# Kernel tuning notes

Measured on AMD Instinct MI355X. Metric: run time of the kernel, lower is better.

The kernel has to match this reference:

```python
import jax, jax.numpy as jnp
import numpy as np

NEG = jnp.float32(-1e9)


def setup_inputs() -> dict:
    key = jax.random.key(0)
    ks = jax.random.split(key, 8)
    B, S, D = 8, 2048, 1024
    scale = 1.0 / np.sqrt(D)
    return {
        "xQ": jax.random.normal(ks[0], (B, S, D), jnp.float32),
        "xK": jax.random.normal(ks[1], (B, S, D), jnp.float32),
        "xV": jax.random.normal(ks[2], (B, S, D), jnp.float32),
        "padding_mask": jax.random.randint(ks[3], (B, S), 0, 2, jnp.int32),
        "casual_mask": jnp.ones((B, S), jnp.int32),
        "W_q": jax.random.normal(ks[4], (D, D), jnp.float32) * scale,
        "b_q": jnp.zeros((D,), jnp.float32),
        "W_k": jax.random.normal(ks[5], (D, D), jnp.float32) * scale,
        "b_k": jnp.zeros((D,), jnp.float32),
        "W_v": jax.random.normal(ks[6], (D, D), jnp.float32) * scale,
        "b_v": jnp.zeros((D,), jnp.float32),
    }


def reference(xQ, xK, xV, padding_mask, casual_mask, W_q, b_q, W_k, b_k, W_v, b_v):
    # Linear projections (torch nn.Linear: x @ W.T + b)
    Q = jnp.einsum('bsd,ed->bse', xQ, W_q) + b_q
    K = jnp.einsum('bsd,ed->bse', xK, W_k) + b_k
    V = jnp.einsum('bsd,ed->bse', xV, W_v) + b_v

    # Raw logits (note: original code applies NO 1/sqrt(dk) scaling)
    QKT = jnp.einsum('bqd,bkd->bqk', Q, K)  # [B, Sq, Sk]

    # Additive padding mask: -1e9 on padded key positions
    pad = jnp.where(padding_mask[:, None, :] == 0, NEG, jnp.float32(0.0))
    # Additive causal mask: -1e9 above the diagonal
    Sq, Sk = QKT.shape[1], QKT.shape[2]
    caus = jnp.where(
        jnp.tril(jnp.ones((Sq, Sk), dtype=bool)), jnp.float32(0.0), NEG
    )[None, :, :]
    QKT = QKT + pad + caus

    S = jax.nn.softmax(QKT, axis=-1)
    return jnp.einsum('bqk,bkd->bqd', S, V)
```

## Files before the change

kernel.cpp:

```cpp
#include <hip/hip_runtime.h>

typedef __attribute__((ext_vector_type(4))) float f4;
typedef __attribute__((ext_vector_type(4))) float f32x4;
typedef _Float16 half8 __attribute__((ext_vector_type(8)));

#define DEVI static __device__ __forceinline__

DEVI void gload_lds16(const void* g, void* l) {
  __builtin_amdgcn_global_load_lds(
      (const __attribute__((address_space(1))) void*)g,
      (__attribute__((address_space(3))) void*)l, 16, 0, 0);
}

DEVI int xcd_swz(int id, int n) {
  int q = n >> 3, r = n & 7;
  int x = id & 7, c = id >> 3;
  return (x < r ? x * (q + 1) : r * (q + 1) + (x - r) * q) + c;
}

#define FENCED_BARRIER()                \
  __builtin_amdgcn_sched_barrier(0);    \
  __builtin_amdgcn_s_barrier();         \
  __builtin_amdgcn_sched_barrier(0);

#define SWZ(kgv, rowv) ((((kgv) ^ ((rowv) >> 1)) & 3) * 8)

__global__ __launch_bounds__(256) void cvt_plain(const float* __restrict__ X,
                                                 _Float16* __restrict__ H,
                                                 int n4) {
  int i = blockIdx.x * 256 + threadIdx.x;
  const int stride = gridDim.x * 256;
  typedef _Float16 half4v __attribute__((ext_vector_type(4)));
  for (; i < n4; i += stride) {
    f4 x = ((const f4*)X)[i];
    half4v h;
#pragma unroll
    for (int j = 0; j < 4; ++j) h[j] = (_Float16)x[j];
    ((half4v*)H)[i] = h;
  }
}

__global__ __launch_bounds__(256) void cvt_split(const float* __restrict__ X,
                                                 _Float16* __restrict__ H,
                                                 _Float16* __restrict__ L,
                                                 int n4) {
  int i = blockIdx.x * 256 + threadIdx.x;
  const int stride = gridDim.x * 256;
  typedef _Float16 half4v __attribute__((ext_vector_type(4)));
  for (; i < n4; i += stride) {
    f4 x = ((const f4*)X)[i];
    half4v h, l;
#pragma unroll
    for (int j = 0; j < 4; ++j) {
      h[j] = (_Float16)x[j];
      l[j] = (_Float16)(x[j] - (float)h[j]);
    }
    ((half4v*)H)[i] = h;
    ((half4v*)L)[i] = l;
  }
}

DEVI void acc_zero44(f32x4 (&acc)[4][4]) {
#pragma unroll
  for (int i = 0; i < 4; ++i)
#pragma unroll
    for (int j = 0; j < 4; ++j) acc[i][j] = (f32x4)0.0f;
}
DEVI void acc_zero42(f32x4 (&acc)[4][2]) {
#pragma unroll
  for (int i = 0; i < 4; ++i)
#pragma unroll
    for (int j = 0; j < 2; ++j) acc[i][j] = (f32x4)0.0f;
}

template <int WSPLIT, int OUTMODE>
__global__ __launch_bounds__(512, 2) void proj_fused(
    const float* __restrict__ X, const _Float16* __restrict__ Wh,
    const _Float16* __restrict__ Wl, const float* __restrict__ bias,
    _Float16* __restrict__ OutHi, _Float16* __restrict__ OutLo,
    _Float16* __restrict__ VtOut) {
  extern __shared__ _Float16 lds[];
  constexpr int ACH = 256 * 32;
  constexpr int BCH = 128 * 32;
  constexpr int CHUNK = ACH + BCH * (1 + WSPLIT);
  const int id = xcd_swz(blockIdx.x, gridDim.x);
  const int m0 = (id >> 3) * 256, n0 = (id & 7) * 128;
  const float* A = X + (size_t)m0 * 1024;
  const _Float16* B0 = Wh + (size_t)n0 * 1024;
  const _Float16* B1 = Wl + (size_t)n0 * 1024;
  const int tid = threadIdx.x;
  const int w = tid >> 6, lane = tid & 63;
  const int wm = w >> 1, wn = w & 1;
  const int r16 = lane & 15, kg = lane >> 4;
  f32x4 acc[4][4];
  acc_zero44(acc);
  f4 ra[4];

  auto ALOAD = [&](int t) {
#pragma unroll
    for (int j = 0; j < 2; ++j) {
      int g = tid + j * 512;
      int row = g >> 2, c = g & 3;
      const float* src = A + (size_t)row * 1024 + t * 32 + c * 8;
      ra[2 * j] = *(const f4*)src;
      ra[2 * j + 1] = *(const f4*)(src + 4);
    }
  };
  auto AWRITE = [&](int buf) {
    _Float16* ab = lds + buf * CHUNK;
#pragma unroll
    for (int j = 0; j < 2; ++j) {
      int g = tid + j * 512;
      int row = g >> 2, c = g & 3;
      half8 h;
#pragma unroll
      for (int e = 0; e < 4; ++e) {
        h[e] = (_Float16)ra[2 * j][e];
        h[e + 4] = (_Float16)ra[2 * j + 1][e];
      }
      *(half8*)(ab + (size_t)row * 32 + SWZ(c, row)) = h;
    }
  };
  auto WLOAD = [&](int t, int buf) {
    _Float16* bb = lds + buf * CHUNK + ACH;
    int row = tid >> 2, c = tid & 3;
    int cs = (c ^ (row >> 1)) & 3;
    gload_lds16(B0 + (size_t)row * 1024 + t * 32 + cs * 8, bb + tid * 8);
    if (WSPLIT)
      gload_lds16(B1 + (size_t)row * 1024 + t * 32 + cs * 8,
                  bb + BCH + tid * 8);
  };
  auto COMPUTE = [&](int buf) {
    const _Float16* la = lds + buf * CHUNK;
    const _Float16* lb = la + ACH;
    half8 a[4], b0f[4], b1f[4];
#pragma unroll
    for (int mi = 0; mi < 4; ++mi) {
      int row = wm * 64 + mi * 16 + r16;
      a[mi] = *(const half8*)(la + row * 32 + SWZ(kg, row));
    }
#pragma unroll
    for (int ni = 0; ni < 4; ++ni) {
      int row = wn * 64 + ni * 16 + r16;
      int off = row * 32 + SWZ(kg, row);
      b0f[ni] = *(const half8*)(lb + off);
      if (WSPLIT) b1f[ni] = *(const half8*)(lb + BCH + off);
    }
    __builtin_amdgcn_s_setprio(1);
#pragma unroll
    for (int mi = 0; mi < 4; ++mi)
#pragma unroll
      for (int ni = 0; ni < 4; ++ni) {
        acc[mi][ni] = __builtin_amdgcn_mfma_f32_16x16x32_f16(
            a[mi], b0f[ni], acc[mi][ni], 0, 0, 0);
        if (WSPLIT)
          acc[mi][ni] = __builtin_amdgcn_mfma_f32_16x16x32_f16(
              a[mi], b1f[ni], acc[mi][ni], 0, 0, 0);
      }
    __builtin_amdgcn_s_setprio(0);
  };

  const int NS = 32;
  WLOAD(0, 0);
  ALOAD(0);
  asm volatile("s_waitcnt vmcnt(0)" ::: "memory");
  __builtin_amdgcn_sched_barrier(0);
  AWRITE(0);
  asm volatile("s_waitcnt lgkmcnt(0)" ::: "memory");
  FENCED_BARRIER();
  for (int t = 0; t < NS; ++t) {
    if (t + 1 < NS) {
      WLOAD(t + 1, (t + 1) & 1);
      ALOAD(t + 1);
    }
    COMPUTE(t & 1);
    if (t + 1 < NS) {
      asm volatile("s_waitcnt vmcnt(0)" ::: "memory");
      __builtin_amdgcn_sched_barrier(0);
      AWRITE((t + 1) & 1);
      asm volatile("s_waitcnt lgkmcnt(0)" ::: "memory");
      FENCED_BARRIER();
    }
  }

  float bcol[4];
#pragma unroll
  for (int ni = 0; ni < 4; ++ni) bcol[ni] = bias[n0 + wn * 64 + ni * 16 + r16];

  if (OUTMODE != 2) {
#pragma unroll
    for (int mi = 0; mi < 4; ++mi) {
      int row = m0 + wm * 64 + mi * 16 + kg * 4;
#pragma unroll
      for (int ni = 0; ni < 4; ++ni) {
        int col = n0 + wn * 64 + ni * 16 + r16;
#pragma unroll
        for (int j = 0; j < 4; ++j) {
          float v = acc[mi][ni][j] + bcol[ni];
          _Float16 h = (_Float16)v;
          OutHi[(size_t)(row + j) * 1024 + col] = h;
          if (OUTMODE == 0)
            OutLo[(size_t)(row + j) * 1024 + col] = (_Float16)(v - (float)h);
        }
      }
    }
  } else {
    __syncthreads();
    _Float16(*T)[256] = (_Float16(*)[256])lds;
#pragma unroll
    for (int mi = 0; mi < 4; ++mi) {
      int ml = wm * 64 + mi * 16 + kg * 4;
#pragma unroll
      for (int ni = 0; ni < 4; ++ni) {
        int nl = wn * 64 + ni * 16 + r16;
#pragma unroll
        for (int j = 0; j < 4; ++j)
          T[nl][ml + j] = (_Float16)(acc[mi][ni][j] + bcol[ni]);
      }
    }
    __syncthreads();
    const int b = m0 >> 11;
    const int s0 = m0 & 2047;
#pragma unroll
    for (int r = 0; r < 8; ++r) {
      int flat = tid + r * 512;
      int n = flat >> 5, c = flat & 31;
      half8 v = *(const half8*)&T[n][c * 8];
      *(half8*)(VtOut + (size_t)b * (1024 * 2048) + (size_t)(n0 + n) * 2048 +
                s0 + c * 8) = v;
    }
  }
}

__global__ __launch_bounds__(512, 4) void qk_eng(
    const _Float16* __restrict__ Qh, const _Float16* __restrict__ Ql,
    const _Float16* __restrict__ Kh, float* __restrict__ Lg, int bbase) {
  extern __shared__ _Float16 lds[];
  constexpr int CHUNK = 12288;
  const int id = xcd_swz(blockIdx.x, gridDim.x);
  const int y = id / 144;
  int t = id % 144;
  int g4 = 0, base = 0;
  while (t >= base + (g4 + 1) * 4) { base += (g4 + 1) * 4; ++g4; }
  const int rem = t - base;
  const int qt = g4 * 4 + rem / (g4 + 1);
  const int kt = rem % (g4 + 1);
  const int b = bbase + y;
  const size_t boff = (size_t)b * (2048 * 1024);
  const _Float16* A0 = Qh + boff + (size_t)(qt * 64) * 1024;
  const _Float16* A1 = Ql + boff + (size_t)(qt * 64) * 1024;
  const _Float16* B0 = Kh + boff + (size_t)(kt * 256) * 1024;
  const int tid = threadIdx.x;
  const int w = tid >> 6, lane = tid & 63;
  const int r16 = lane & 15, kg = lane >> 4;
  const int wn = w;
  f32x4 acc[4][2];
  acc_zero42(acc);

  auto STAGE = [&](int t_, int buf) {
    _Float16* base_ = lds + buf * CHUNK;
    {
      int g = tid & 255;
      int row = g >> 2, c = g & 3;
      int cs = (c ^ (row >> 1)) & 3;
      const _Float16* src = (tid < 256) ? A0 : A1;
      _Float16* dst = base_ + ((tid < 256) ? 0 : 2048);
      gload_lds16(src + (size_t)row * 1024 + t_ * 32 + cs * 8, dst + g * 8);
    }
#pragma unroll
    for (int j = 0; j < 2; ++j) {
      int g = tid + j * 512;
      int row = g >> 2, c = g & 3;
      int cs = (c ^ (row >> 1)) & 3;
      gload_lds16(B0 + (size_t)row * 1024 + t_ * 32 + cs * 8,
                  base_ + 4096 + g * 8);
    }
  };
  auto COMPUTE = [&](int buf) {
    const _Float16* la = lds + buf * CHUNK;
    half8 a0[4], a1[4], bf[2];
#pragma unroll
    for (int mi = 0; mi < 4; ++mi) {
      int row = mi * 16 + r16;
      int off = row * 32 + SWZ(kg, row);
      a0[mi] = *(const half8*)(la + off);
      a1[mi] = *(const half8*)(la + 2048 + off);
    }
#pragma unroll
    for (int ni = 0; ni < 2; ++ni) {
      int row = wn * 32 + ni * 16 + r16;
      bf[ni] = *(const half8*)(la + 4096 + row * 32 + SWZ(kg, row));
    }
    __builtin_amdgcn_s_setprio(1);
#pragma unroll
    for (int mi = 0; mi < 4; ++mi)
#pragma unroll
      for (int ni = 0; ni < 2; ++ni) {
        acc[mi][ni] = __builtin_amdgcn_mfma_f32_16x16x32_f16(
            a0[mi], bf[ni], acc[mi][ni], 0, 0, 0);
        acc[mi][ni] = __builtin_amdgcn_mfma_f32_16x16x32_f16(
            a1[mi], bf[ni], acc[mi][ni], 0, 0, 0);
      }
    __builtin_amdgcn_s_setprio(0);
  };

  const int NS = 32;
  STAGE(0, 0);
  STAGE(1, 1);
  int tt = 0;
  for (; tt < NS - 1; ++tt) {
    asm volatile("s_waitcnt vmcnt(3)" ::: "memory");
    FENCED_BARRIER();
    if (tt + 2 < NS) STAGE(tt + 2, (tt + 2) % 3);
    COMPUTE(tt % 3);
  }
  asm volatile("s_waitcnt vmcnt(0)" ::: "memory");
  FENCED_BARRIER();
  COMPUTE(tt % 3);

  float* L = Lg + (size_t)y * (2048 * 2048);
#pragma unroll
  for (int mi = 0; mi < 4; ++mi) {
    int row = qt * 64 + mi * 16 + kg * 4;
#pragma unroll
    for (int ni = 0; ni < 2; ++ni) {
      int col = kt * 256 + wn * 32 + ni * 16 + r16;
#pragma unroll
      for (int j = 0; j < 4; ++j)
        L[(size_t)(row + j) * 2048 + col] = acc[mi][ni][j];
    }
  }
}

__global__ __launch_bounds__(512, 4) void pv_eng(
    const float* __restrict__ Lg, const _Float16* __restrict__ Vt,
    float* __restrict__ Out, int bbase) {
  extern __shared__ _Float16 lds[];
  constexpr int CHUNK = 8192;
  const int id = xcd_swz(blockIdx.x, gridDim.x);
  const int y = id >> 7;
  const int qt = (id & 127) >> 3, nt = id & 7;
  const int b = bbase + y;
  const _Float16* P = (const _Float16*)(Lg + (size_t)y * (2048 * 2048));
  const _Float16* A0 = P + (size_t)(qt * 128) * 4096;
  const _Float16* B0 =
      Vt + (size_t)b * (1024 * 2048) + (size_t)(nt * 128) * 2048;
  const int NS = (qt + 1) * 4;
  const int tid = threadIdx.x;
  const int w = tid >> 6, lane = tid & 63;
  const int wm = w >> 2, wn = w & 3;
  const int r16 = lane & 15, kg = lane >> 4;
  f32x4 acc[4][2];
  acc_zero42(acc);

  auto STAGE = [&](int t_, int buf) {
    _Float16* base_ = lds + buf * CHUNK;
    {
      int row = tid >> 2, c = tid & 3;
      int cs = (c ^ (row >> 1)) & 3;
      gload_lds16(A0 + (size_t)row * 4096 + t_ * 32 + cs * 8, base_ + tid * 8);
      gload_lds16(B0 + (size_t)row * 2048 + t_ * 32 + cs * 8,
                  base_ + 4096 + tid * 8);
    }
  };
  auto COMPUTE = [&](int buf) {
    const _Float16* la = lds + buf * CHUNK;
    half8 a[4], bf[2];
#pragma unroll
    for (int mi = 0; mi < 4; ++mi) {
      int row = wm * 64 + mi * 16 + r16;
      a[mi] = *(const half8*)(la + row * 32 + SWZ(kg, row));
    }
#pragma unroll
    for (int ni = 0; ni < 2; ++ni) {
      int row = wn * 32 + ni * 16 + r16;
      bf[ni] = *(const half8*)(la + 4096 + row * 32 + SWZ(kg, row));
    }
    __builtin_amdgcn_s_setprio(1);
#pragma unroll
    for (int mi = 0; mi < 4; ++mi)
#pragma unroll
      for (int ni = 0; ni < 2; ++ni)
        acc[mi][ni] = __builtin_amdgcn_mfma_f32_16x16x32_f16(
            a[mi], bf[ni], acc[mi][ni], 0, 0, 0);
    __builtin_amdgcn_s_setprio(0);
  };

  STAGE(0, 0);
  STAGE(1, 1);
  int tt = 0;
  for (; tt < NS - 1; ++tt) {
    asm volatile("s_waitcnt vmcnt(2)" ::: "memory");
    FENCED_BARRIER();
    if (tt + 2 < NS) STAGE(tt + 2, (tt + 2) % 3);
    COMPUTE(tt % 3);
  }
  asm volatile("s_waitcnt vmcnt(0)" ::: "memory");
  FENCED_BARRIER();
  COMPUTE(tt % 3);

#pragma unroll
  for (int mi = 0; mi < 4; ++mi) {
    int row = qt * 128 + wm * 64 + mi * 16 + kg * 4;
#pragma unroll
    for (int ni = 0; ni < 2; ++ni) {
      int col = nt * 128 + wn * 32 + ni * 16 + r16;
#pragma unroll
      for (int j = 0; j < 4; ++j)
        Out[(size_t)(b * 2048 + row + j) * 1024 + col] = acc[mi][ni][j];
    }
  }
}

__global__ __launch_bounds__(256) void softmax_kernel(
    float* __restrict__ Lg, const int* __restrict__ pad, int bbase) {
  const int q = blockIdx.x;
  const int y = blockIdx.y;
  const int b = bbase + y;
  const int tid = threadIdx.x;
  float* row = Lg + (size_t)y * (2048 * 2048) + (size_t)q * 2048;
  _Float16* prow = (_Float16*)row;
  const int* pb = pad + (size_t)b * 2048;
  const int kend = ((q >> 8) + 1) << 8;
  float v[8];
  int nv = 0;
  float mx = -3.0e38f;
  for (int k = tid; k <= q; k += 256) {
    float l = row[k];
    if (pb[k] == 0) l += -1.0e9f;
    v[nv++] = l;
    mx = fmaxf(mx, l);
  }
  __shared__ float red[4];
  for (int o = 32; o; o >>= 1) mx = fmaxf(mx, __shfl_xor(mx, o));
  if ((tid & 63) == 0) red[tid >> 6] = mx;
  __syncthreads();
  mx = fmaxf(fmaxf(red[0], red[1]), fmaxf(red[2], red[3]));
  __syncthreads();
  float s = 0.f;
  for (int i = 0; i < nv; ++i) s += expf(v[i] - mx);
  for (int o = 32; o; o >>= 1) s += __shfl_xor(s, o);
  if ((tid & 63) == 0) red[tid >> 6] = s;
  __syncthreads();
  s = red[0] + red[1] + red[2] + red[3];
  const float inv = 1.0f / s;
  int i = 0;
  for (int k = tid; k <= q; k += 256) {
    prow[k] = (_Float16)(expf(v[i] - mx) * inv);
    ++i;
  }
  for (int k = q + 1 + tid; k < kend; k += 256) prow[k] = (_Float16)0.0f;
}

__global__ __launch_bounds__(512) void fix_f(const int* __restrict__ pad,
                                             int* __restrict__ fb) {
  const int b = threadIdx.x >> 6, k = threadIdx.x & 63;
  unsigned long long m = __ballot(pad[b * 2048 + k] != 0);
  if (k == 0) fb[b] = m ? (__ffsll((long long)m) - 1) : 64;
}

__global__ __launch_bounds__(256) void fix_qrow2(
    const float* __restrict__ xQ, const float* __restrict__ Wq,
    const float* __restrict__ bq, const int* __restrict__ fb,
    float* __restrict__ Qrow) {
  const int b = blockIdx.y;
  const int f = fb[b];
  const int tid = threadIdx.x;
  const int e = blockIdx.x * 16 + (tid >> 4);
  const int l16 = tid & 15;
  __shared__ float xq[1024];
  for (int q = 0; q < f; ++q) {
    *(f4*)&xq[tid * 4] = ((const f4*)(xQ + (size_t)(b * 2048 + q) * 1024))[tid];
    __syncthreads();
    float a = 0.f;
#pragma unroll
    for (int it = 0; it < 16; ++it) {
      int d = l16 * 4 + it * 64;
      f4 ww = *(const f4*)(Wq + (size_t)e * 1024 + d);
      a += xq[d] * ww[0] + xq[d + 1] * ww[1] + xq[d + 2] * ww[2] +
           xq[d + 3] * ww[3];
    }
    for (int o = 8; o; o >>= 1) a += __shfl_xor(a, o);
    if (l16 == 0) Qrow[((size_t)b * 64 + q) * 1024 + e] = a + bq[e];
    __syncthreads();
  }
}

__global__ __launch_bounds__(256) void fix_qb0(const float* __restrict__ bk,
                                               const int* __restrict__ fb,
                                               const float* __restrict__ Qrow,
                                               float* __restrict__ qb0) {
  const int q = blockIdx.x, b = blockIdx.y;
  if (q >= fb[b]) return;
  const int tid = threadIdx.x;
  const float* qr = Qrow + ((size_t)b * 64 + q) * 1024;
  float p = 0.f;
  for (int e = tid; e < 1024; e += 256) p += qr[e] * bk[e];
  __shared__ float red[4];
  for (int o = 32; o; o >>= 1) p += __shfl_xor(p, o);
  if ((tid & 63) == 0) red[tid >> 6] = p;
  __syncthreads();
  if (tid == 0) qb0[b * 64 + q] = red[0] + red[1] + red[2] + red[3];
}

__global__ __launch_bounds__(256) void fix_g2(const float* __restrict__ Wk,
                                              const int* __restrict__ fb,
                                              const float* __restrict__ Qrow,
                                              float* __restrict__ Gpart) {
  const int b = blockIdx.y;
  const int f = fb[b];
  const int tid = threadIdx.x;
  const int ddblk = blockIdx.x & 3, es = blockIdx.x >> 2;
  const int dd = ddblk * 256 + tid;
  __shared__ float qc[128];
  for (int q = 0; q < f; ++q) {
    if (tid < 32)
      *(f4*)&qc[tid * 4] =
          ((const f4*)(Qrow + ((size_t)b * 64 + q) * 1024 + es * 128))[tid];
    __syncthreads();
    float g = 0.f;
    for (int e = 0; e < 128; ++e)
      g += qc[e] * Wk[(size_t)(es * 128 + e) * 1024 + dd];
    Gpart[(((size_t)es * 8 + b) * 64 + q) * 1024 + dd] = g;
    __syncthreads();
  }
}

__global__ __launch_bounds__(256) void fix_logit2(
    const float* __restrict__ xK, const int* __restrict__ pad,
    const int* __restrict__ fb, const float* __restrict__ Gpart,
    const float* __restrict__ qb0, float* __restrict__ lrow) {
  const int b = blockIdx.y;
  const int f = fb[b];
  const int tid = threadIdx.x;
  const int k = blockIdx.x * 16 + (tid >> 4);
  const int l16 = tid & 15;
  __shared__ float Gs[1024];
  for (int q = 0; q < f; ++q) {
    f4 s = (f4)0.0f;
#pragma unroll
    for (int es = 0; es < 8; ++es)
      s += ((const f4*)(Gpart + (((size_t)es * 8 + b) * 64 + q) * 1024))[tid];
    *(f4*)&Gs[tid * 4] = s;
    __syncthreads();
    float a = 0.f;
#pragma unroll
    for (int it = 0; it < 16; ++it) {
      int d = l16 * 4 + it * 64;
      f4 x = *(const f4*)(xK + (size_t)(b * 2048 + k) * 1024 + d);
      a += x[0] * Gs[d] + x[1] * Gs[d + 1] + x[2] * Gs[d + 2] +
           x[3] * Gs[d + 3];
    }
    for (int o = 8; o; o >>= 1) a += __shfl_xor(a, o);
    if (l16 == 0) {
      float l = a + qb0[b * 64 + q];
      if (pad[b * 2048 + k] == 0) l += -1.0e9f;
      if (k > q) l += -1.0e9f;
      lrow[((size_t)b * 64 + q) * 2048 + k] = l;
    }
    __syncthreads();
  }
}

__global__ __launch_bounds__(256) void fix_sm(const int* __restrict__ fb,
                                              float* __restrict__ lrow,
                                              float* __restrict__ srow) {
  const int q = blockIdx.x, b = blockIdx.y;
  if (q >= fb[b]) return;
  const int tid = threadIdx.x;
  float* row = lrow + ((size_t)b * 64 + q) * 2048;
  float v[8];
  float mx = -3.0e38f;
#pragma unroll
  for (int i = 0; i < 8; ++i) {
    v[i] = row[tid + i * 256];
    mx = fmaxf(mx, v[i]);
  }
  __shared__ float red[4];
  for (int o = 32; o; o >>= 1) mx = fmaxf(mx, __shfl_xor(mx, o));
  if ((tid & 63) == 0) red[tid >> 6] = mx;
  __syncthreads();
  mx = fmaxf(fmaxf(red[0], red[1]), fmaxf(red[2], red[3]));
  __syncthreads();
  float s = 0.f;
#pragma unroll
  for (int i = 0; i < 8; ++i) {
    v[i] = expf(v[i] - mx);
    s += v[i];
  }
#pragma unroll
  for (int i = 0; i < 8; ++i) row[tid + i * 256] = v[i];
  for (int o = 32; o; o >>= 1) s += __shfl_xor(s, o);
  if ((tid & 63) == 0) red[tid >> 6] = s;
  __syncthreads();
  if (tid == 0) srow[b * 64 + q] = red[0] + red[1] + red[2] + red[3];
}

__global__ __launch_bounds__(256) void fix_pv2(
    const _Float16* __restrict__ Vt, const int* __restrict__ fb,
    const float* __restrict__ lrow, const float* __restrict__ srow,
    float* __restrict__ Out) {
  const int b = blockIdx.y;
  const int f = fb[b];
  const int tid = threadIdx.x;
  const int d = blockIdx.x * 16 + (tid >> 4);
  const int l16 = tid & 15;
  __shared__ float ps[2048];
  for (int q = 0; q < f; ++q) {
    const f4* src = (const f4*)(lrow + ((size_t)b * 64 + q) * 2048);
    *(f4*)&ps[tid * 8] = src[tid * 2];
    *(f4*)&ps[tid * 8 + 4] = src[tid * 2 + 1];
    __syncthreads();
    float o = 0.f;
#pragma unroll
    for (int it = 0; it < 16; ++it) {
      int k = l16 * 8 + it * 128;
      half8 vv = *(const half8*)(Vt + (size_t)b * (1024 * 2048) +
                                 (size_t)d * 2048 + k);
      o += (float)vv[0] * ps[k] + (float)vv[1] * ps[k + 1] +
           (float)vv[2] * ps[k + 2] + (float)vv[3] * ps[k + 3] +
           (float)vv[4] * ps[k + 4] + (float)vv[5] * ps[k + 5] +
           (float)vv[6] * ps[k + 6] + (float)vv[7] * ps[k + 7];
    }
    for (int of = 8; of; of >>= 1) o += __shfl_xor(o, of);
    if (l16 == 0)
      Out[(size_t)(b * 2048 + q) * 1024 + d] = o * (1.0f / srow[b * 64 + q]);
    __syncthreads();
  }
}

extern "C" void kernel_launch(void* const* d_in, const int* in_sizes, int n_in,
                              void* d_out, int out_size, void* d_ws,
                              size_t ws_size, hipStream_t stream) {
  const float* xQ = (const float*)d_in[0];
  const float* xK = (const float*)d_in[1];
  const float* xV = (const float*)d_in[2];
  const int* pad = (const int*)d_in[3];
  const float* Wq = (const float*)d_in[5];
  const float* bq = (const float*)d_in[6];
  const float* Wk = (const float*)d_in[7];
  const float* bk = (const float*)d_in[8];
  const float* Wv = (const float*)d_in[9];
  const float* bv = (const float*)d_in[10];
  float* Out = (float*)d_out;

  const size_t MB = (size_t)1 << 20;
  char* wsb = (char*)d_ws;
  _Float16* Qh = (_Float16*)(wsb);
  _Float16* Ql = (_Float16*)(wsb + 32 * MB);
  _Float16* Kh = (_Float16*)(wsb + 64 * MB);
  _Float16* Vt = (_Float16*)(wsb + 96 * MB);
  float* Lg = (float*)(wsb + 128 * MB);

  size_t avail = (ws_size > 128 * MB) ? ws_size - 128 * MB : 0;
  int G = (int)(avail / (16 * MB));
  if (G > 8) G = 8;
  if (G < 1) G = 1;

  _Float16* Wqh = (_Float16*)(wsb + 128 * MB);
  _Float16* Wql = (_Float16*)(wsb + 130 * MB);
  _Float16* Wkh = (_Float16*)(wsb + 132 * MB);
  _Float16* Wkl = (_Float16*)(wsb + 134 * MB);
  _Float16* Wvh = (_Float16*)(wsb + 136 * MB);

  const int SM_P = 65536;
  const int SM_V = 65536;
  const int SM_QK = 73728;
  const int SM_PV = 49152;
  (void)hipFuncSetAttribute((const void*)&proj_fused<1, 0>,
                            hipFuncAttributeMaxDynamicSharedMemorySize, SM_P);
  (void)hipFuncSetAttribute((const void*)&proj_fused<1, 1>,
                            hipFuncAttributeMaxDynamicSharedMemorySize, SM_P);
  (void)hipFuncSetAttribute((const void*)&proj_fused<0, 2>,
                            hipFuncAttributeMaxDynamicSharedMemorySize, SM_V);
  (void)hipFuncSetAttribute((const void*)&qk_eng,
                            hipFuncAttributeMaxDynamicSharedMemorySize, SM_QK);
  (void)hipFuncSetAttribute((const void*)&pv_eng,
                            hipFuncAttributeMaxDynamicSharedMemorySize, SM_PV);

  dim3 blk(256), eblk(512);

  cvt_split<<<dim3(1024), blk, 0, stream>>>(Wq, Wqh, Wql, 262144);
  cvt_split<<<dim3(1024), blk, 0, stream>>>(Wk, Wkh, Wkl, 262144);
  cvt_plain<<<dim3(1024), blk, 0, stream>>>(Wv, Wvh, 262144);

  proj_fused<0, 2><<<dim3(512), eblk, SM_V, stream>>>(xV, Wvh, Wvh, bv,
                                                      nullptr, nullptr, Vt);
  proj_fused<1, 1><<<dim3(512), eblk, SM_P, stream>>>(xK, Wkh, Wkl, bk, Kh,
                                                      nullptr, nullptr);
  proj_fused<1, 0><<<dim3(512), eblk, SM_P, stream>>>(xQ, Wqh, Wql, bq, Qh, Ql,
                                                      nullptr);

  for (int bbase = 0; bbase < 8; bbase += G) {
    int nb = (8 - bbase < G) ? (8 - bbase) : G;
    qk_eng<<<dim3(144 * nb), eblk, SM_QK, stream>>>(Qh, Ql, Kh, Lg, bbase);
    softmax_kernel<<<dim3(2048, nb), blk, 0, stream>>>(Lg, pad, bbase);
    pv_eng<<<dim3(128 * nb), eblk, SM_PV, stream>>>(Lg, Vt, Out, bbase);
  }

  int* fb = (int*)(wsb);
  float* qb0 = (float*)(wsb + 4 * 1024);
  float* srow = (float*)(wsb + 8 * 1024);
  float* Qrow = (float*)(wsb + 1 * MB);
  float* Gpart = (float*)(wsb + 4 * MB);
  float* lrow = (float*)(wsb + 20 * MB);

  fix_f<<<dim3(1), dim3(512), 0, stream>>>(pad, fb);
  fix_qrow2<<<dim3(64, 8), blk, 0, stream>>>(xQ, Wq, bq, fb, Qrow);
  fix_qb0<<<dim3(64, 8), blk, 0, stream>>>(bk, fb, Qrow, qb0);
  fix_g2<<<dim3(32, 8), blk, 0, stream>>>(Wk, fb, Qrow, Gpart);
  fix_logit2<<<dim3(128, 8), blk, 0, stream>>>(xK, pad, fb, Gpart, qb0, lrow);
  fix_sm<<<dim3(64, 8), blk, 0, stream>>>(fb, lrow, srow);
  fix_pv2<<<dim3(64, 8), blk, 0, stream>>>(Vt, fb, lrow, srow, Out);
}
```

Baseline: 547.5 us.

## Pre-convert activations to fp16 and restructure projection, PV and masking pipelines

The X inputs are now converted to fp16 in separate kernels, so the projection GEMMs can stream both operands with direct global-to-LDS loads through a 3-stage pipeline on 128x128 tiles. The weight conversions are merged into one launch. The padding mask moves from softmax into the QK epilogue. pv_eng now uses 256-thread blocks with 128x128 tiles, and each block takes a pair of causal tiles (front and back) to balance triangular work. Batch chunking is spread evenly across launches. This adds extra fp16 activation write and read traffic and more workspace use, in exchange for a simpler, better-overlapped GEMM main loop.

New measurement: 496.8 us. 1.1x faster.

```diff
diff --git a/kernel.cpp b/kernel.cpp
--- a/kernel.cpp
+++ b/kernel.cpp
@@ -25,39 +25,72 @@
 
 #define SWZ(kgv, rowv) ((((kgv) ^ ((rowv) >> 1)) & 3) * 8)
 
+typedef _Float16 half4v __attribute__((ext_vector_type(4)));
+
+DEVI void cvt_plain_body(const float* X, _Float16* H, int n4, int i,
+                         int stride) {
+  for (; i < n4; i += stride) {
+    f4 x = ((const f4*)X)[i];
+    half4v h;
+#pragma unroll
+    for (int j = 0; j < 4; ++j) h[j] = (_Float16)x[j];
+    ((half4v*)H)[i] = h;
+  }
+}
+DEVI void cvt_split_body(const float* X, _Float16* H, _Float16* L, int n4,
+                         int i, int stride) {
+  for (; i < n4; i += stride) {
+    f4 x = ((const f4*)X)[i];
+    half4v h, l;
+#pragma unroll
+    for (int j = 0; j < 4; ++j) {
+      h[j] = (_Float16)x[j];
+      l[j] = (_Float16)(x[j] - (float)h[j]);
+    }
+    ((half4v*)H)[i] = h;
+    ((half4v*)L)[i] = l;
+  }
+}
+
 __global__ __launch_bounds__(256) void cvt_plain(const float* __restrict__ X,
                                                  _Float16* __restrict__ H,
                                                  int n4) {
-  int i = blockIdx.x * 256 + threadIdx.x;
-  const int stride = gridDim.x * 256;
-  typedef _Float16 half4v __attribute__((ext_vector_type(4)));
-  for (; i < n4; i += stride) {
-    f4 x = ((const f4*)X)[i];
-    half4v h;
-#pragma unroll
-    for (int j = 0; j < 4; ++j) h[j] = (_Float16)x[j];
-    ((half4v*)H)[i] = h;
-  }
+  cvt_plain_body(X, H, n4, blockIdx.x * 256 + threadIdx.x, gridDim.x * 256);
 }
 
 __global__ __launch_bounds__(256) void cvt_split(const float* __restrict__ X,
                                                  _Float16* __restrict__ H,
                                                  _Float16* __restrict__ L,
                                                  int n4) {
-  int i = blockIdx.x * 256 + threadIdx.x;
+  cvt_split_body(X, H, L, n4, blockIdx.x * 256 + threadIdx.x,
+                 gridDim.x * 256);
+}
+
+__global__ __launch_bounds__(256) void cvt_w_all(
+    const float* __restrict__ Wq, const float* __restrict__ Wk,
+    const float* __restrict__ Wv, _Float16* __restrict__ Wqh,
+    _Float16* __restrict__ Wql, _Float16* __restrict__ Wkh,
+    _Float16* __restrict__ Wkl, _Float16* __restrict__ Wvh) {
+  const int i = blockIdx.x * 256 + threadIdx.x;
   const int stride = gridDim.x * 256;
-  typedef _Float16 half4v __attribute__((ext_vector_type(4)));
-  for (; i < n4; i += stride) {
-    f4 x = ((const f4*)X)[i];
-    half4v h, l;
-#pragma unroll
-    for (int j = 0; j < 4; ++j) {
-      h[j] = (_Float16)x[j];
-      l[j] = (_Float16)(x[j] - (float)h[j]);
-    }
-    ((half4v*)H)[i] = h;
-    ((half4v*)L)[i] = l;
-  }
+  if (blockIdx.y == 0)
+    cvt_split_body(Wq, Wqh, Wql, 262144, i, stride);
+  else if (blockIdx.y == 1)
+    cvt_split_body(Wk, Wkh, Wkl, 262144, i, stride);
+  else
+    cvt_plain_body(Wv, Wvh, 262144, i, stride);
+}
+
+__global__ __launch_bounds__(256) void cvt_x_kq(const float* __restrict__ xK,
+                                                const float* __restrict__ xQ,
+                                                _Float16* __restrict__ Hk,
+                                                _Float16* __restrict__ Hq) {
+  const int i = blockIdx.x * 256 + threadIdx.x;
+  const int stride = gridDim.x * 256;
+  if (blockIdx.y == 0)
+    cvt_plain_body(xK, Hk, 4194304, i, stride);
+  else
+    cvt_plain_body(xQ, Hq, 4194304, i, stride);
 }
 
 DEVI void acc_zero44(f32x4 (&acc)[4][4]) {
@@ -74,18 +107,18 @@
 }
 
 template <int WSPLIT, int OUTMODE>
-__global__ __launch_bounds__(512, 2) void proj_fused(
-    const float* __restrict__ X, const _Float16* __restrict__ Wh,
+__global__ __launch_bounds__(256, 2) void proj3(
+    const _Float16* __restrict__ X, const _Float16* __restrict__ Wh,
     const _Float16* __restrict__ Wl, const float* __restrict__ bias,
     _Float16* __restrict__ OutHi, _Float16* __restrict__ OutLo,
     _Float16* __restrict__ VtOut) {
   extern __shared__ _Float16 lds[];
-  constexpr int ACH = 256 * 32;
+  constexpr int ACH = 128 * 32;
   constexpr int BCH = 128 * 32;
   constexpr int CHUNK = ACH + BCH * (1 + WSPLIT);
   const int id = xcd_swz(blockIdx.x, gridDim.x);
-  const int m0 = (id >> 3) * 256, n0 = (id & 7) * 128;
-  const float* A = X + (size_t)m0 * 1024;
+  const int m0 = (id >> 3) * 128, n0 = (id & 7) * 128;
+  const _Float16* A0 = X + (size_t)m0 * 1024;
   const _Float16* B0 = Wh + (size_t)n0 * 1024;
   const _Float16* B1 = Wl + (size_t)n0 * 1024;
   const int tid = threadIdx.x;
@@ -94,41 +127,19 @@
   const int r16 = lane & 15, kg = lane >> 4;
   f32x4 acc[4][4];
   acc_zero44(acc);
-  f4 ra[4];
-
-  auto ALOAD = [&](int t) {
+
+  auto STAGE = [&](int t, int buf) {
+    _Float16* base = lds + buf * CHUNK;
 #pragma unroll
     for (int j = 0; j < 2; ++j) {
-      int g = tid + j * 512;
+      int g = tid + j * 256;
       int row = g >> 2, c = g & 3;
-      const float* src = A + (size_t)row * 1024 + t * 32 + c * 8;
-      ra[2 * j] = *(const f4*)src;
-      ra[2 * j + 1] = *(const f4*)(src + 4);
-    }
-  };
-  auto AWRITE = [&](int buf) {
-    _Float16* ab = lds + buf * CHUNK;
-#pragma unroll
-    for (int j = 0; j < 2; ++j) {
-      int g = tid + j * 512;
-      int row = g >> 2, c = g & 3;
-      half8 h;
-#pragma unroll
-      for (int e = 0; e < 4; ++e) {
-        h[e] = (_Float16)ra[2 * j][e];
-        h[e + 4] = (_Float16)ra[2 * j + 1][e];
-      }
-      *(half8*)(ab + (size_t)row * 32 + SWZ(c, row)) = h;
-    }
-  };
-  auto WLOAD = [&](int t, int buf) {
-    _Float16* bb = lds + buf * CHUNK + ACH;
-    int row = tid >> 2, c = tid & 3;
-    int cs = (c ^ (row >> 1)) & 3;
-    gload_lds16(B0 + (size_t)row * 1024 + t * 32 + cs * 8, bb + tid * 8);
-    if (WSPLIT)
-      gload_lds16(B1 + (size_t)row * 1024 + t * 32 + cs * 8,
-                  bb + BCH + tid * 8);
+      int cs = (c ^ (row >> 1)) & 3;
+      size_t src = (size_t)row * 1024 + t * 32 + cs * 8;
+      gload_lds16(A0 + src, base + g * 8);
+      gload_lds16(B0 + src, base + ACH + g * 8);
+      if (WSPLIT) gload_lds16(B1 + src, base + ACH + BCH + g * 8);
+    }
   };
   auto COMPUTE = [&](int buf) {
     const _Float16* la = lds + buf * CHUNK;
@@ -161,27 +172,21 @@
   };
 
   const int NS = 32;
-  WLOAD(0, 0);
-  ALOAD(0);
+  STAGE(0, 0);
+  STAGE(1, 1);
+  int tt = 0;
+  for (; tt < NS - 1; ++tt) {
+    if constexpr (WSPLIT)
+      asm volatile("s_waitcnt vmcnt(6)" ::: "memory");
+    else
+      asm volatile("s_waitcnt vmcnt(4)" ::: "memory");
+    FENCED_BARRIER();
+    if (tt + 2 < NS) STAGE(tt + 2, (tt + 2) % 3);
+    COMPUTE(tt % 3);
+  }
   asm volatile("s_waitcnt vmcnt(0)" ::: "memory");
-  __builtin_amdgcn_sched_barrier(0);
-  AWRITE(0);
-  asm volatile("s_waitcnt lgkmcnt(0)" ::: "memory");
   FENCED_BARRIER();
-  for (int t = 0; t < NS; ++t) {
-    if (t + 1 < NS) {
-      WLOAD(t + 1, (t + 1) & 1);
-      ALOAD(t + 1);
-    }
-    COMPUTE(t & 1);
-    if (t + 1 < NS) {
-      asm volatile("s_waitcnt vmcnt(0)" ::: "memory");
-      __builtin_amdgcn_sched_barrier(0);
-      AWRITE((t + 1) & 1);
-      asm volatile("s_waitcnt lgkmcnt(0)" ::: "memory");
-      FENCED_BARRIER();
-    }
-  }
+  COMPUTE(tt % 3);
 
   float bcol[4];
 #pragma unroll
@@ -206,7 +211,7 @@
     }
   } else {
     __syncthreads();
-    _Float16(*T)[256] = (_Float16(*)[256])lds;
+    _Float16(*T)[128] = (_Float16(*)[128])lds;
 #pragma unroll
     for (int mi = 0; mi < 4; ++mi) {
       int ml = wm * 64 + mi * 16 + kg * 4;
@@ -223,8 +228,8 @@
     const int s0 = m0 & 2047;
 #pragma unroll
     for (int r = 0; r < 8; ++r) {
-      int flat = tid + r * 512;
-      int n = flat >> 5, c = flat & 31;
+      int flat = tid + r * 256;
+      int n = flat >> 4, c = flat & 15;
       half8 v = *(const half8*)&T[n][c * 8];
       *(half8*)(VtOut + (size_t)b * (1024 * 2048) + (size_t)(n0 + n) * 2048 +
                 s0 + c * 8) = v;
@@ -234,7 +239,8 @@
 
 __global__ __launch_bounds__(512, 4) void qk_eng(
     const _Float16* __restrict__ Qh, const _Float16* __restrict__ Ql,
-    const _Float16* __restrict__ Kh, float* __restrict__ Lg, int bbase) {
+    const _Float16* __restrict__ Kh, const int* __restrict__ pad,
+    float* __restrict__ Lg, int bbase) {
   extern __shared__ _Float16 lds[];
   constexpr int CHUNK = 12288;
   const int id = xcd_swz(blockIdx.x, gridDim.x);
@@ -319,115 +325,124 @@
   COMPUTE(tt % 3);
 
   float* L = Lg + (size_t)y * (2048 * 2048);
-#pragma unroll
-  for (int mi = 0; mi < 4; ++mi) {
-    int row = qt * 64 + mi * 16 + kg * 4;
-#pragma unroll
-    for (int ni = 0; ni < 2; ++ni) {
-      int col = kt * 256 + wn * 32 + ni * 16 + r16;
+  const int* pb = pad + (size_t)b * 2048;
+#pragma unroll
+  for (int ni = 0; ni < 2; ++ni) {
+    int col = kt * 256 + wn * 32 + ni * 16 + r16;
+    const float padd = (pb[col] == 0) ? -1.0e9f : 0.0f;
+#pragma unroll
+    for (int mi = 0; mi < 4; ++mi) {
+      int row = qt * 64 + mi * 16 + kg * 4;
 #pragma unroll
       for (int j = 0; j < 4; ++j)
-        L[(size_t)(row + j) * 2048 + col] = acc[mi][ni][j];
-    }
-  }
-}
-
-__global__ __launch_bounds__(512, 4) void pv_eng(
+        L[(size_t)(row + j) * 2048 + col] = acc[mi][ni][j] + padd;
+    }
+  }
+}
+
+__global__ __launch_bounds__(256, 3) void pv_eng(
     const float* __restrict__ Lg, const _Float16* __restrict__ Vt,
-    float* __restrict__ Out, int bbase) {
+    float* __restrict__ Out, int bbase, int ntiles) {
   extern __shared__ _Float16 lds[];
   constexpr int CHUNK = 8192;
-  const int id = xcd_swz(blockIdx.x, gridDim.x);
-  const int y = id >> 7;
-  const int qt = (id & 127) >> 3, nt = id & 7;
-  const int b = bbase + y;
-  const _Float16* P = (const _Float16*)(Lg + (size_t)y * (2048 * 2048));
-  const _Float16* A0 = P + (size_t)(qt * 128) * 4096;
-  const _Float16* B0 =
-      Vt + (size_t)b * (1024 * 2048) + (size_t)(nt * 128) * 2048;
-  const int NS = (qt + 1) * 4;
+  const int g0 = xcd_swz(blockIdx.x, gridDim.x);
   const int tid = threadIdx.x;
   const int w = tid >> 6, lane = tid & 63;
-  const int wm = w >> 2, wn = w & 3;
+  const int wm = w >> 1, wn = w & 1;
   const int r16 = lane & 15, kg = lane >> 4;
-  f32x4 acc[4][2];
-  acc_zero42(acc);
-
-  auto STAGE = [&](int t_, int buf) {
-    _Float16* base_ = lds + buf * CHUNK;
-    {
-      int row = tid >> 2, c = tid & 3;
-      int cs = (c ^ (row >> 1)) & 3;
-      gload_lds16(A0 + (size_t)row * 4096 + t_ * 32 + cs * 8, base_ + tid * 8);
-      gload_lds16(B0 + (size_t)row * 2048 + t_ * 32 + cs * 8,
-                  base_ + 4096 + tid * 8);
-    }
-  };
-  auto COMPUTE = [&](int buf) {
-    const _Float16* la = lds + buf * CHUNK;
-    half8 a[4], bf[2];
+
+  for (int half = 0; half < 2; ++half) {
+    const int idt = half ? (ntiles - 1 - g0) : g0;
+    const int y = idt >> 7;
+    const int qt = (idt & 127) >> 3, nt = idt & 7;
+    const int b = bbase + y;
+    const _Float16* P = (const _Float16*)(Lg + (size_t)y * (2048 * 2048));
+    const _Float16* A0 = P + (size_t)(qt * 128) * 4096;
+    const _Float16* B0 =
+        Vt + (size_t)b * (1024 * 2048) + (size_t)(nt * 128) * 2048;
+    const int NS = (qt + 1) * 4;
+    f32x4 acc[4][4];
+    acc_zero44(acc);
+
+    auto STAGE = [&](int t_, int buf) {
+      _Float16* base_ = lds + buf * CHUNK;
+#pragma unroll
+      for (int j = 0; j < 2; ++j) {
+        int g = tid + j * 256;
+        int row = g >> 2, c = g & 3;
+        int cs = (c ^ (row >> 1)) & 3;
+        gload_lds16(A0 + (size_t)row * 4096 + t_ * 32 + cs * 8, base_ + g * 8);
+        gload_lds16(B0 + (size_t)row * 2048 + t_ * 32 + cs * 8,
+                    base_ + 4096 + g * 8);
+      }
+    };
+    auto COMPUTE = [&](int buf) {
+      const _Float16* la = lds + buf * CHUNK;
+      half8 a[4], bf[4];
+#pragma unroll
+      for (int mi = 0; mi < 4; ++mi) {
+        int row = wm * 64 + mi * 16 + r16;
+        a[mi] = *(const half8*)(la + row * 32 + SWZ(kg, row));
+      }
+#pragma unroll
+      for (int ni = 0; ni < 4; ++ni) {
+        int row = wn * 64 + ni * 16 + r16;
+        bf[ni] = *(const half8*)(la + 4096 + row * 32 + SWZ(kg, row));
+      }
+      __builtin_amdgcn_s_setprio(1);
+#pragma unroll
+      for (int mi = 0; mi < 4; ++mi)
+#pragma unroll
+        for (int ni = 0; ni < 4; ++ni)
+          acc[mi][ni] = __builtin_amdgcn_mfma_f32_16x16x32_f16(
+              a[mi], bf[ni], acc[mi][ni], 0, 0, 0);
+      __builtin_amdgcn_s_setprio(0);
+    };
+
+    STAGE(0, 0);
+    STAGE(1, 1);
+    int tt = 0;
+    for (; tt < NS - 1; ++tt) {
+      asm volatile("s_waitcnt vmcnt(4)" ::: "memory");
+      FENCED_BARRIER();
+      if (tt + 2 < NS) STAGE(tt + 2, (tt + 2) % 3);
+      COMPUTE(tt % 3);
+    }
+    asm volatile("s_waitcnt vmcnt(0)" ::: "memory");
+    FENCED_BARRIER();
+    COMPUTE(tt % 3);
+
 #pragma unroll
     for (int mi = 0; mi < 4; ++mi) {
-      int row = wm * 64 + mi * 16 + r16;
-      a[mi] = *(const half8*)(la + row * 32 + SWZ(kg, row));
-    }
-#pragma unroll
-    for (int ni = 0; ni < 2; ++ni) {
-      int row = wn * 32 + ni * 16 + r16;
-      bf[ni] = *(const half8*)(la + 4096 + row * 32 + SWZ(kg, row));
-    }
-    __builtin_amdgcn_s_setprio(1);
-#pragma unroll
-    for (int mi = 0; mi < 4; ++mi)
-#pragma unroll
-      for (int ni = 0; ni < 2; ++ni)
-        acc[mi][ni] = __builtin_amdgcn_mfma_f32_16x16x32_f16(
-            a[mi], bf[ni], acc[mi][ni], 0, 0, 0);
-    __builtin_amdgcn_s_setprio(0);
-  };
-
-  STAGE(0, 0);
-  STAGE(1, 1);
-  int tt = 0;
-  for (; tt < NS - 1; ++tt) {
-    asm volatile("s_waitcnt vmcnt(2)" ::: "memory");
-    FENCED_BARRIER();
-    if (tt + 2 < NS) STAGE(tt + 2, (tt + 2) % 3);
-    COMPUTE(tt % 3);
-  }
-  asm volatile("s_waitcnt vmcnt(0)" ::: "memory");
-  FENCED_BARRIER();
-  COMPUTE(tt % 3);
-
-#pragma unroll
-  for (int mi = 0; mi < 4; ++mi) {
-    int row = qt * 128 + wm * 64 + mi * 16 + kg * 4;
-#pragma unroll
-    for (int ni = 0; ni < 2; ++ni) {
-      int col = nt * 128 + wn * 32 + ni * 16 + r16;
-#pragma unroll
-      for (int j = 0; j < 4; ++j)
-        Out[(size_t)(b * 2048 + row + j) * 1024 + col] = acc[mi][ni][j];
-    }
-  }
-}
-
-__global__ __launch_bounds__(256) void softmax_kernel(
-    float* __restrict__ Lg, const int* __restrict__ pad, int bbase) {
+      int row = qt * 128 + wm * 64 + mi * 16 + kg * 4;
+#pragma unroll
+      for (int ni = 0; ni < 4; ++ni) {
+        int col = nt * 128 + wn * 64 + ni * 16 + r16;
+#pragma unroll
+        for (int j = 0; j < 4; ++j)
+          Out[(size_t)(b * 2048 + row + j) * 1024 + col] = acc[mi][ni][j];
+      }
+    }
+    if (half == 0) {
+      asm volatile("s_waitcnt vmcnt(0) lgkmcnt(0)" ::: "memory");
+      FENCED_BARRIER();
+    }
+  }
+}
+
+__global__ __launch_bounds__(256) void softmax_kernel(float* __restrict__ Lg,
+                                                      int bbase) {
   const int q = blockIdx.x;
   const int y = blockIdx.y;
-  const int b = bbase + y;
   const int tid = threadIdx.x;
   float* row = Lg + (size_t)y * (2048 * 2048) + (size_t)q * 2048;
   _Float16* prow = (_Float16*)row;
-  const int* pb = pad + (size_t)b * 2048;
   const int kend = ((q >> 8) + 1) << 8;
   float v[8];
   int nv = 0;
   float mx = -3.0e38f;
   for (int k = tid; k <= q; k += 256) {
     float l = row[k];
-    if (pb[k] == 0) l += -1.0e9f;
     v[nv++] = l;
     mx = fmaxf(mx, l);
   }
@@ -656,23 +671,19 @@
   int G = (int)(avail / (16 * MB));
   if (G > 8) G = 8;
   if (G < 1) G = 1;
-
-  _Float16* Wqh = (_Float16*)(wsb + 128 * MB);
-  _Float16* Wql = (_Float16*)(wsb + 130 * MB);
-  _Float16* Wkh = (_Float16*)(wsb + 132 * MB);
-  _Float16* Wkl = (_Float16*)(wsb + 134 * MB);
-  _Float16* Wvh = (_Float16*)(wsb + 136 * MB);
-
-  const int SM_P = 65536;
-  const int SM_V = 65536;
+  int nchunks = (8 + G - 1) / G;
+  int base_nb = 8 / nchunks, extra = 8 % nchunks;
+
+  const int SM_P1 = 73728;
+  const int SM_P0 = 73728;
   const int SM_QK = 73728;
   const int SM_PV = 49152;
-  (void)hipFuncSetAttribute((const void*)&proj_fused<1, 0>,
-                            hipFuncAttributeMaxDynamicSharedMemorySize, SM_P);
-  (void)hipFuncSetAttribute((const void*)&proj_fused<1, 1>,
-                            hipFuncAttributeMaxDynamicSharedMemorySize, SM_P);
-  (void)hipFuncSetAttribute((const void*)&proj_fused<0, 2>,
-                            hipFuncAttributeMaxDynamicSharedMemorySize, SM_V);
+  (void)hipFuncSetAttribute((const void*)&proj3<1, 0>,
+                            hipFuncAttributeMaxDynamicSharedMemorySize, SM_P1);
+  (void)hipFuncSetAttribute((const void*)&proj3<1, 1>,
+                            hipFuncAttributeMaxDynamicSharedMemorySize, SM_P1);
+  (void)hipFuncSetAttribute((const void*)&proj3<0, 2>,
+                            hipFuncAttributeMaxDynamicSharedMemorySize, SM_P0);
   (void)hipFuncSetAttribute((const void*)&qk_eng,
                             hipFuncAttributeMaxDynamicSharedMemorySize, SM_QK);
   (void)hipFuncSetAttribute((const void*)&pv_eng,
@@ -680,22 +691,55 @@
 
   dim3 blk(256), eblk(512);
 
-  cvt_split<<<dim3(1024), blk, 0, stream>>>(Wq, Wqh, Wql, 262144);
-  cvt_split<<<dim3(1024), blk, 0, stream>>>(Wk, Wkh, Wkl, 262144);
-  cvt_plain<<<dim3(1024), blk, 0, stream>>>(Wv, Wvh, 262144);
-
-  proj_fused<0, 2><<<dim3(512), eblk, SM_V, stream>>>(xV, Wvh, Wvh, bv,
-                                                      nullptr, nullptr, Vt);
-  proj_fused<1, 1><<<dim3(512), eblk, SM_P, stream>>>(xK, Wkh, Wkl, bk, Kh,
-                                                      nullptr, nullptr);
-  proj_fused<1, 0><<<dim3(512), eblk, SM_P, stream>>>(xQ, Wqh, Wql, bq, Qh, Ql,
-                                                      nullptr);
-
-  for (int bbase = 0; bbase < 8; bbase += G) {
-    int nb = (8 - bbase < G) ? (8 - bbase) : G;
-    qk_eng<<<dim3(144 * nb), eblk, SM_QK, stream>>>(Qh, Ql, Kh, Lg, bbase);
-    softmax_kernel<<<dim3(2048, nb), blk, 0, stream>>>(Lg, pad, bbase);
-    pv_eng<<<dim3(128 * nb), eblk, SM_PV, stream>>>(Lg, Vt, Out, bbase);
+  _Float16* Wvh = (_Float16*)(wsb + 160 * MB);
+  _Float16* Wkh = (_Float16*)(wsb + 162 * MB);
+  _Float16* Wkl = (_Float16*)(wsb + 164 * MB);
+  _Float16* Wqh = (_Float16*)(wsb + 166 * MB);
+  _Float16* Wql = (_Float16*)(wsb + 168 * MB);
+  _Float16* sXvk = (_Float16*)(wsb);
+  _Float16* sXq = (_Float16*)(wsb + 128 * MB);
+
+  if (ws_size >= 170 * MB) {
+    cvt_w_all<<<dim3(1024, 3), blk, 0, stream>>>(Wq, Wk, Wv, Wqh, Wql, Wkh,
+                                                 Wkl, Wvh);
+    cvt_plain<<<dim3(2048), blk, 0, stream>>>(xV, sXvk, 4194304);
+    proj3<0, 2><<<dim3(1024), blk, SM_P0, stream>>>(sXvk, Wvh, Wvh, bv,
+                                                    nullptr, nullptr, Vt);
+    cvt_x_kq<<<dim3(2048, 2), blk, 0, stream>>>(xK, xQ, sXvk, sXq);
+    proj3<1, 1><<<dim3(1024), blk, SM_P1, stream>>>(sXvk, Wkh, Wkl, bk, Kh,
+                                                    nullptr, nullptr);
+    proj3<1, 0><<<dim3(1024), blk, SM_P1, stream>>>(sXq, Wqh, Wql, bq, Qh, Ql,
+                                                    nullptr);
+  } else {
+    _Float16* fWh = (_Float16*)(wsb + 32 * MB);
+    _Float16* fWl = (_Float16*)(wsb + 34 * MB);
+    cvt_plain<<<dim3(2048), blk, 0, stream>>>(xV, sXvk, 4194304);
+    cvt_plain<<<dim3(1024), blk, 0, stream>>>(Wv, fWh, 262144);
+    proj3<0, 2><<<dim3(1024), blk, SM_P0, stream>>>(sXvk, fWh, fWh, bv,
+                                                    nullptr, nullptr, Vt);
+    cvt_plain<<<dim3(2048), blk, 0, stream>>>(xK, sXvk, 4194304);
+    cvt_split<<<dim3(1024), blk, 0, stream>>>(Wk, fWh, fWl, 262144);
+    proj3<1, 1><<<dim3(1024), blk, SM_P1, stream>>>(sXvk, fWh, fWl, bk, Kh,
+                                                    nullptr, nullptr);
+    cvt_plain<<<dim3(2048), blk, 0, stream>>>(xQ, sXq, 4194304);
+    cvt_split<<<dim3(1024), blk, 0, stream>>>(Wq, (_Float16*)(wsb + 160 * MB),
+                                              (_Float16*)(wsb + 162 * MB),
+                                              262144);
+    proj3<1, 0><<<dim3(1024), blk, SM_P1, stream>>>(
+        sXq, (_Float16*)(wsb + 160 * MB), (_Float16*)(wsb + 162 * MB), bq, Qh,
+        Ql, nullptr);
+  }
+
+  int bbase = 0;
+  for (int c = 0; c < nchunks; ++c) {
+    int nb = base_nb + (c < extra ? 1 : 0);
+    if (nb <= 0) break;
+    qk_eng<<<dim3(144 * nb), eblk, SM_QK, stream>>>(Qh, Ql, Kh, pad, Lg,
+                                                    bbase);
+    softmax_kernel<<<dim3(2048, nb), blk, 0, stream>>>(Lg, bbase);
+    pv_eng<<<dim3(64 * nb), blk, SM_PV, stream>>>(Lg, Vt, Out, bbase,
+                                                  128 * nb);
+    bbase += nb;
   }
 
   int* fb = (int*)(wsb);
```
